# Kernel optimization log

Hardware: AMD Instinct MI355X
Metric: run time of the kernel (lower is better)

The kernel has to match this reference:

```python
import jax, jax.numpy as jnp
import numpy as np

B, S, H = 4096, 64, 256
NUM_STEPS = 200
DT = 0.01


def setup_inputs() -> dict:
    key = jax.random.key(0)
    ks = jax.random.split(key, 7)
    sc = lambda fan_in: 1.0 / np.sqrt(fan_in)
    return {
        "x0": jax.random.normal(ks[0], (B, S), dtype=jnp.float32),
        "W1": jax.random.normal(ks[1], (S, H), dtype=jnp.float32) * sc(S),
        "b1": jax.random.normal(ks[2], (H,), dtype=jnp.float32) * sc(S),
        "W2": jax.random.normal(ks[3], (H, H), dtype=jnp.float32) * sc(H),
        "b2": jax.random.normal(ks[4], (H,), dtype=jnp.float32) * sc(H),
        "W3": jax.random.normal(ks[5], (H, S), dtype=jnp.float32) * sc(H),
        "b3": jax.random.normal(ks[6], (S,), dtype=jnp.float32) * sc(H),
        "dt_scale": jnp.ones((1,), dtype=jnp.float32) * 0.01,
        "num_steps": NUM_STEPS,
    }


def reference(x0, W1, b1, W2, b2, W3, b3, dt_scale, num_steps):
    # Euler integration of dx/dt = MLP(x); trajectory = [x0, x1, ..., x_num_steps]
    def step(x, _):
        h = jnp.tanh(x @ W1 + b1)          # [B, H]
        h = jnp.tanh(h @ W2 + b2)          # [B, H]
        dx_dt = h @ W3 + b3                # [B, S]
        x_next = x + dx_dt * dt_scale * DT
        return x_next, x_next

    _, traj = jax.lax.scan(step, x0, None, length=num_steps)  # [T, B, S]
    traj = jnp.moveaxis(traj, 0, 1)                            # [B, T, S]
    return jnp.concatenate([x0[:, None, :], traj], axis=1)     # [B, T+1, S]
```

## Files before the change

kernel.cpp:

```cpp
#include <hip/hip_runtime.h>
#include <hip/hip_bf16.h>

typedef __bf16 bf16x8 __attribute__((ext_vector_type(8)));
typedef __bf16 bf16x4 __attribute__((ext_vector_type(4)));
typedef float  f32x4  __attribute__((ext_vector_type(4)));

__device__ __forceinline__ float fast_tanh(float x) {
    float e = __expf(2.0f * x);
    float r = __builtin_amdgcn_rcpf(e + 1.0f);
    return __builtin_fmaf(-2.0f, r, 1.0f);
}

__global__ void prep_weights(const float* __restrict__ W1,
                             const float* __restrict__ W2,
                             const float* __restrict__ W3,
                             __bf16* __restrict__ w1t,
                             __bf16* __restrict__ w2t,
                             __bf16* __restrict__ w3t) {
    int idx = blockIdx.x * blockDim.x + threadIdx.x;
    if (idx < 64 * 256) {
        int n = idx >> 6, k = idx & 63;
        w1t[idx] = (__bf16)W1[k * 256 + n];
    }
    int i2 = idx - 64 * 256;
    if (i2 >= 0 && i2 < 256 * 256) {
        int n = i2 >> 8, k = i2 & 255;
        w2t[i2] = (__bf16)W2[k * 256 + n];
    }
    int i3 = idx - 64 * 256 - 256 * 256;
    if (i3 >= 0 && i3 < 64 * 256) {
        int n = i3 >> 8, k = i3 & 255;
        w3t[i3] = (__bf16)W3[k * 64 + n];
    }
}

__global__ __launch_bounds__(1024, 4)
void ode_kernel(const float* __restrict__ x0,
                const float* __restrict__ b1,
                const float* __restrict__ b2,
                const float* __restrict__ b3,
                const float* __restrict__ dt_scale,
                const int*   __restrict__ num_steps,
                const __bf16* __restrict__ w1t,
                const __bf16* __restrict__ w2t,
                const __bf16* __restrict__ w3t,
                float* __restrict__ out) {
    __shared__ __bf16 xb[16][72];
    __shared__ __align__(16) __bf16 h1[16 * 256];
    __shared__ __align__(16) __bf16 h2[16 * 256];

    const int tid  = threadIdx.x;
    const int wave = tid >> 6;
    const int lane = tid & 63;
    const int q    = lane >> 4;
    const int c    = lane & 15;
    const int cx8  = (c & 7) << 3;
    const int row0 = blockIdx.x * 16;

    const float scale = dt_scale[0] * 0.01f;
    const int   nT    = num_steps[0];

    const int nw = wave * 16 + c;

    bf16x8 w1f[2];
    #pragma unroll
    for (int kt = 0; kt < 2; ++kt)
        w1f[kt] = *(const bf16x8*)(w1t + nw * 64 + kt * 32 + q * 8);
    bf16x8 w2f[8];
    #pragma unroll
    for (int kt = 0; kt < 8; ++kt)
        w2f[kt] = *(const bf16x8*)(w2t + nw * 256 + kt * 32 + q * 8);

    f32x4 b1v = *(const f32x4*)(b1 + wave * 16 + q * 4);
    f32x4 b2v = *(const f32x4*)(b2 + wave * 16 + q * 4);

    bf16x8 w3f[8];
    f32x4  b3v = (f32x4){0.f, 0.f, 0.f, 0.f};
    f32x4  xv  = (f32x4){0.f, 0.f, 0.f, 0.f};
    float* outp = out;
    if (wave < 4) {
        #pragma unroll
        for (int kt = 0; kt < 8; ++kt)
            w3f[kt] = *(const bf16x8*)(w3t + nw * 256 + kt * 32 + q * 8);
        b3v = *(const f32x4*)(b3 + wave * 16 + q * 4);
        xv = *(const f32x4*)(x0 + (size_t)(row0 + c) * 64 + wave * 16 + q * 4);
        outp = out + (size_t)(row0 + c) * 201 * 64 + wave * 16 + q * 4;
        *(f32x4*)outp = xv;
        outp += 64;
        bf16x4 xbv;
        #pragma unroll
        for (int r = 0; r < 4; ++r) xbv[r] = (__bf16)xv[r];
        *(bf16x4*)(&xb[c][wave * 16 + q * 4]) = xbv;
    }
    __syncthreads();

    for (int t = 0; t < nT; ++t) {
        {
            f32x4 acc = b1v;
            #pragma unroll
            for (int kt = 0; kt < 2; ++kt) {
                bf16x8 a = *(const bf16x8*)(&xb[c][kt * 32 + q * 8]);
                acc = __builtin_amdgcn_mfma_f32_16x16x32_bf16(w1f[kt], a, acc, 0, 0, 0);
            }
            bf16x4 o;
            #pragma unroll
            for (int r = 0; r < 4; ++r) o[r] = (__bf16)fast_tanh(acc[r]);
            *(bf16x4*)(&h1[c * 256 + ((wave * 16 + q * 4) ^ cx8)]) = o;
        }
        __syncthreads();

        {
            f32x4 acc  = b2v;
            f32x4 accB = (f32x4){0, 0, 0, 0};
            #pragma unroll
            for (int kt = 0; kt < 4; ++kt) {
                bf16x8 a0 = *(const bf16x8*)(&h1[c * 256 + ((kt * 32 + q * 8) ^ cx8)]);
                bf16x8 a1 = *(const bf16x8*)(&h1[c * 256 + (((kt + 4) * 32 + q * 8) ^ cx8)]);
                acc  = __builtin_amdgcn_mfma_f32_16x16x32_bf16(w2f[kt],     a0, acc,  0, 0, 0);
                accB = __builtin_amdgcn_mfma_f32_16x16x32_bf16(w2f[kt + 4], a1, accB, 0, 0, 0);
            }
            f32x4 s = acc + accB;
            bf16x4 o;
            #pragma unroll
            for (int r = 0; r < 4; ++r) o[r] = (__bf16)fast_tanh(s[r]);
            *(bf16x4*)(&h2[c * 256 + ((wave * 16 + q * 4) ^ cx8)]) = o;
        }
        __syncthreads();

        if (wave < 4) {
            f32x4 acc  = b3v;
            f32x4 accB = (f32x4){0, 0, 0, 0};
            #pragma unroll
            for (int kt = 0; kt < 4; ++kt) {
                bf16x8 a0 = *(const bf16x8*)(&h2[c * 256 + ((kt * 32 + q * 8) ^ cx8)]);
                bf16x8 a1 = *(const bf16x8*)(&h2[c * 256 + (((kt + 4) * 32 + q * 8) ^ cx8)]);
                acc  = __builtin_amdgcn_mfma_f32_16x16x32_bf16(w3f[kt],     a0, acc,  0, 0, 0);
                accB = __builtin_amdgcn_mfma_f32_16x16x32_bf16(w3f[kt + 4], a1, accB, 0, 0, 0);
            }
            acc += accB;
            xv += acc * scale;
            bf16x4 xbv;
            #pragma unroll
            for (int r = 0; r < 4; ++r) xbv[r] = (__bf16)xv[r];
            *(bf16x4*)(&xb[c][wave * 16 + q * 4]) = xbv;
            *(f32x4*)outp = xv;
            outp += 64;
        }
        __syncthreads();
    }
}

extern "C" void kernel_launch(void* const* d_in, const int* in_sizes, int n_in,
                              void* d_out, int out_size, void* d_ws, size_t ws_size,
                              hipStream_t stream) {
    const float* x0 = (const float*)d_in[0];
    const float* W1 = (const float*)d_in[1];
    const float* b1 = (const float*)d_in[2];
    const float* W2 = (const float*)d_in[3];
    const float* b2 = (const float*)d_in[4];
    const float* W3 = (const float*)d_in[5];
    const float* b3 = (const float*)d_in[6];
    const float* dt = (const float*)d_in[7];
    const int*   ns = (const int*)d_in[8];

    __bf16* w1t = (__bf16*)d_ws;
    __bf16* w2t = w1t + 64 * 256;
    __bf16* w3t = w2t + 256 * 256;

    prep_weights<<<384, 256, 0, stream>>>(W1, W2, W3, w1t, w2t, w3t);

    int rows = in_sizes[0] / 64;
    ode_kernel<<<rows / 16, 1024, 0, stream>>>(x0, b1, b2, b3, dt, ns,
                                               w1t, w2t, w3t, (float*)d_out);
}
```

Before: 464.3 us.

## Use 4 waves per block with 4 N-tiles each and raw barriers

Shrinks each block from 16 waves to 4. Each wave now computes four 16-column output tiles for layers 1 and 2, which keeps 4x more weight fragments in registers and reuses each LDS activation load across four MFMAs. The XOR swizzle is replaced by padded LDS rows, and __syncthreads is replaced by an inline-asm waitcnt+s_barrier. The intent is to cut barrier cost and LDS reads per MFMA. In exchange, register use per thread rises sharply (about 40 bf16x8 weight fragments), which may spill or limit occupancy, and there are fewer waves to hide latency.

```diff
diff --git a/kernel.cpp b/kernel.cpp
--- a/kernel.cpp
+++ b/kernel.cpp
@@ -4,6 +4,8 @@
 typedef __bf16 bf16x8 __attribute__((ext_vector_type(8)));
 typedef __bf16 bf16x4 __attribute__((ext_vector_type(4)));
 typedef float  f32x4  __attribute__((ext_vector_type(4)));
+
+#define BAR() asm volatile("s_waitcnt lgkmcnt(0)\n\ts_barrier" ::: "memory")
 
 __device__ __forceinline__ float fast_tanh(float x) {
     float e = __expf(2.0f * x);
@@ -34,7 +36,7 @@
     }
 }
 
-__global__ __launch_bounds__(1024, 4)
+__global__ __launch_bounds__(256, 1)
 void ode_kernel(const float* __restrict__ x0,
                 const float* __restrict__ b1,
                 const float* __restrict__ b2,
@@ -46,96 +48,122 @@
                 const __bf16* __restrict__ w3t,
                 float* __restrict__ out) {
     __shared__ __bf16 xb[16][72];
-    __shared__ __align__(16) __bf16 h1[16 * 256];
-    __shared__ __align__(16) __bf16 h2[16 * 256];
+    __shared__ __bf16 h1[16][264];
+    __shared__ __bf16 h2[16][264];
 
     const int tid  = threadIdx.x;
     const int wave = tid >> 6;
     const int lane = tid & 63;
     const int q    = lane >> 4;
     const int c    = lane & 15;
-    const int cx8  = (c & 7) << 3;
     const int row0 = blockIdx.x * 16;
 
     const float scale = dt_scale[0] * 0.01f;
     const int   nT    = num_steps[0];
 
-    const int nw = wave * 16 + c;
-
-    bf16x8 w1f[2];
+    bf16x8 w1f[2][4];
     #pragma unroll
     for (int kt = 0; kt < 2; ++kt)
-        w1f[kt] = *(const bf16x8*)(w1t + nw * 64 + kt * 32 + q * 8);
-    bf16x8 w2f[8];
+        #pragma unroll
+        for (int nt = 0; nt < 4; ++nt) {
+            int n = wave * 64 + nt * 16 + c;
+            w1f[kt][nt] = *(const bf16x8*)(w1t + n * 64 + kt * 32 + q * 8);
+        }
+    bf16x8 w2f[8][4];
     #pragma unroll
     for (int kt = 0; kt < 8; ++kt)
-        w2f[kt] = *(const bf16x8*)(w2t + nw * 256 + kt * 32 + q * 8);
-
-    f32x4 b1v = *(const f32x4*)(b1 + wave * 16 + q * 4);
-    f32x4 b2v = *(const f32x4*)(b2 + wave * 16 + q * 4);
-
+        #pragma unroll
+        for (int nt = 0; nt < 4; ++nt) {
+            int n = wave * 64 + nt * 16 + c;
+            w2f[kt][nt] = *(const bf16x8*)(w2t + n * 256 + kt * 32 + q * 8);
+        }
     bf16x8 w3f[8];
-    f32x4  b3v = (f32x4){0.f, 0.f, 0.f, 0.f};
-    f32x4  xv  = (f32x4){0.f, 0.f, 0.f, 0.f};
-    float* outp = out;
-    if (wave < 4) {
+    {
+        int n = wave * 16 + c;
         #pragma unroll
         for (int kt = 0; kt < 8; ++kt)
-            w3f[kt] = *(const bf16x8*)(w3t + nw * 256 + kt * 32 + q * 8);
-        b3v = *(const f32x4*)(b3 + wave * 16 + q * 4);
-        xv = *(const f32x4*)(x0 + (size_t)(row0 + c) * 64 + wave * 16 + q * 4);
-        outp = out + (size_t)(row0 + c) * 201 * 64 + wave * 16 + q * 4;
-        *(f32x4*)outp = xv;
-        outp += 64;
+            w3f[kt] = *(const bf16x8*)(w3t + n * 256 + kt * 32 + q * 8);
+    }
+
+    f32x4 b1v[4], b2v[4];
+    #pragma unroll
+    for (int nt = 0; nt < 4; ++nt) {
+        b1v[nt] = *(const f32x4*)(b1 + wave * 64 + nt * 16 + q * 4);
+        b2v[nt] = *(const f32x4*)(b2 + wave * 64 + nt * 16 + q * 4);
+    }
+    const f32x4 b3v = *(const f32x4*)(b3 + wave * 16 + q * 4);
+
+    f32x4 xv = *(const f32x4*)(x0 + (size_t)(row0 + c) * 64 + wave * 16 + q * 4);
+    float* outp = out + (size_t)(row0 + c) * 201 * 64 + wave * 16 + q * 4;
+    *(f32x4*)outp = xv;
+    outp += 64;
+    {
         bf16x4 xbv;
         #pragma unroll
         for (int r = 0; r < 4; ++r) xbv[r] = (__bf16)xv[r];
         *(bf16x4*)(&xb[c][wave * 16 + q * 4]) = xbv;
     }
-    __syncthreads();
+    BAR();
 
     for (int t = 0; t < nT; ++t) {
         {
-            f32x4 acc = b1v;
-            #pragma unroll
-            for (int kt = 0; kt < 2; ++kt) {
-                bf16x8 a = *(const bf16x8*)(&xb[c][kt * 32 + q * 8]);
-                acc = __builtin_amdgcn_mfma_f32_16x16x32_bf16(w1f[kt], a, acc, 0, 0, 0);
+            bf16x8 xa[2];
+            #pragma unroll
+            for (int kt = 0; kt < 2; ++kt)
+                xa[kt] = *(const bf16x8*)(&xb[c][kt * 32 + q * 8]);
+            f32x4 acc[4] = {b1v[0], b1v[1], b1v[2], b1v[3]};
+            #pragma unroll
+            for (int kt = 0; kt < 2; ++kt)
+                #pragma unroll
+                for (int nt = 0; nt < 4; ++nt)
+                    acc[nt] = __builtin_amdgcn_mfma_f32_16x16x32_bf16(w1f[kt][nt], xa[kt], acc[nt], 0, 0, 0);
+            #pragma unroll
+            for (int nt = 0; nt < 4; ++nt) {
+                bf16x4 o;
+                #pragma unroll
+                for (int r = 0; r < 4; ++r) o[r] = (__bf16)fast_tanh(acc[nt][r]);
+                *(bf16x4*)(&h1[c][wave * 64 + nt * 16 + q * 4]) = o;
             }
-            bf16x4 o;
-            #pragma unroll
-            for (int r = 0; r < 4; ++r) o[r] = (__bf16)fast_tanh(acc[r]);
-            *(bf16x4*)(&h1[c * 256 + ((wave * 16 + q * 4) ^ cx8)]) = o;
-        }
-        __syncthreads();
+        }
+        BAR();
 
         {
-            f32x4 acc  = b2v;
-            f32x4 accB = (f32x4){0, 0, 0, 0};
-            #pragma unroll
-            for (int kt = 0; kt < 4; ++kt) {
-                bf16x8 a0 = *(const bf16x8*)(&h1[c * 256 + ((kt * 32 + q * 8) ^ cx8)]);
-                bf16x8 a1 = *(const bf16x8*)(&h1[c * 256 + (((kt + 4) * 32 + q * 8) ^ cx8)]);
-                acc  = __builtin_amdgcn_mfma_f32_16x16x32_bf16(w2f[kt],     a0, acc,  0, 0, 0);
-                accB = __builtin_amdgcn_mfma_f32_16x16x32_bf16(w2f[kt + 4], a1, accB, 0, 0, 0);
+            bf16x8 f[8];
+            #pragma unroll
+            for (int kt = 0; kt < 8; ++kt)
+                f[kt] = *(const bf16x8*)(&h1[c][kt * 32 + q * 8]);
+            f32x4 acc[4]  = {b2v[0], b2v[1], b2v[2], b2v[3]};
+            f32x4 accB[4] = {(f32x4){0,0,0,0}, (f32x4){0,0,0,0},
+                             (f32x4){0,0,0,0}, (f32x4){0,0,0,0}};
+            #pragma unroll
+            for (int kt = 0; kt < 4; ++kt)
+                #pragma unroll
+                for (int nt = 0; nt < 4; ++nt) {
+                    acc[nt]  = __builtin_amdgcn_mfma_f32_16x16x32_bf16(w2f[kt][nt],     f[kt],     acc[nt],  0, 0, 0);
+                    accB[nt] = __builtin_amdgcn_mfma_f32_16x16x32_bf16(w2f[kt + 4][nt], f[kt + 4], accB[nt], 0, 0, 0);
+                }
+            #pragma unroll
+            for (int nt = 0; nt < 4; ++nt) {
+                f32x4 s = acc[nt] + accB[nt];
+                bf16x4 o;
+                #pragma unroll
+                for (int r = 0; r < 4; ++r) o[r] = (__bf16)fast_tanh(s[r]);
+                *(bf16x4*)(&h2[c][wave * 64 + nt * 16 + q * 4]) = o;
             }
-            f32x4 s = acc + accB;
-            bf16x4 o;
-            #pragma unroll
-            for (int r = 0; r < 4; ++r) o[r] = (__bf16)fast_tanh(s[r]);
-            *(bf16x4*)(&h2[c * 256 + ((wave * 16 + q * 4) ^ cx8)]) = o;
-        }
-        __syncthreads();
-
-        if (wave < 4) {
+        }
+        BAR();
+
+        {
+            bf16x8 g[8];
+            #pragma unroll
+            for (int kt = 0; kt < 8; ++kt)
+                g[kt] = *(const bf16x8*)(&h2[c][kt * 32 + q * 8]);
             f32x4 acc  = b3v;
             f32x4 accB = (f32x4){0, 0, 0, 0};
             #pragma unroll
             for (int kt = 0; kt < 4; ++kt) {
-                bf16x8 a0 = *(const bf16x8*)(&h2[c * 256 + ((kt * 32 + q * 8) ^ cx8)]);
-                bf16x8 a1 = *(const bf16x8*)(&h2[c * 256 + (((kt + 4) * 32 + q * 8) ^ cx8)]);
-                acc  = __builtin_amdgcn_mfma_f32_16x16x32_bf16(w3f[kt],     a0, acc,  0, 0, 0);
-                accB = __builtin_amdgcn_mfma_f32_16x16x32_bf16(w3f[kt + 4], a1, accB, 0, 0, 0);
+                acc  = __builtin_amdgcn_mfma_f32_16x16x32_bf16(w3f[kt],     g[kt],     acc,  0, 0, 0);
+                accB = __builtin_amdgcn_mfma_f32_16x16x32_bf16(w3f[kt + 4], g[kt + 4], accB, 0, 0, 0);
             }
             acc += accB;
             xv += acc * scale;
@@ -146,7 +174,7 @@
             *(f32x4*)outp = xv;
             outp += 64;
         }
-        __syncthreads();
+        BAR();
     }
 }
 
@@ -170,6 +198,6 @@
     prep_weights<<<384, 256, 0, stream>>>(W1, W2, W3, w1t, w2t, w3t);
 
     int rows = in_sizes[0] / 64;
-    ode_kernel<<<rows / 16, 1024, 0, stream>>>(x0, b1, b2, b3, dt, ns,
-                                               w1t, w2t, w3t, (float*)d_out);
-}
+    ode_kernel<<<rows / 16, 256, 0, stream>>>(x0, b1, b2, b3, dt, ns,
+                                              w1t, w2t, w3t, (float*)d_out);
+}
```

Measured after the change: 509.9 us. 1.1x slower.
